# Kernel tuning notes

Hardware: AMD Instinct MI355X
Metric: run time of the kernel (lower is better)

## Reference

```python
import jax, jax.numpy as jnp
import numpy as np

N, E = 50000, 640000          # nodes, edges
F_IN, HID, CLS = 128, 128, 64  # feature dims


def setup_inputs() -> dict:
    key = jax.random.key(0)
    ks = jax.random.split(key, 12)
    x = jax.random.normal(ks[0], (N, F_IN), dtype=jnp.float32)
    edge_index = jax.random.randint(ks[1], (2, E), 0, N, dtype=jnp.int32)
    s_in = 1.0 / np.sqrt(F_IN)
    s_h = 1.0 / np.sqrt(HID)
    return {
        "x": x,
        "edge_index": edge_index,
        "W0": jax.random.normal(ks[2], (F_IN, HID), jnp.float32) * s_in,
        "b0": jnp.zeros((HID,), jnp.float32),
        "W1": jax.random.normal(ks[3], (HID, HID), jnp.float32) * s_h,
        "b1": jnp.zeros((HID,), jnp.float32),
        "W2": jax.random.normal(ks[4], (HID, HID), jnp.float32) * s_h,
        "b2": jnp.zeros((HID,), jnp.float32),
        "W_lin": jax.random.normal(ks[5], (HID, CLS), jnp.float32) * s_h,
        "b_lin": jnp.zeros((CLS,), jnp.float32),
    }


def reference(x, edge_index, W0, b0, W1, b1, W2, b2, W_lin, b_lin):
    # GCNConv (PyG defaults): out = D^-1/2 (A + I) D^-1/2 (x @ W) + b
    row, col = edge_index[0], edge_index[1]  # source -> target
    # degree with self-loop (graph is fixed across layers, compute norms once)
    deg = jnp.zeros((N,), x.dtype).at[col].add(1.0) + 1.0
    dinv = jax.lax.rsqrt(deg)                 # deg >= 1, safe
    enorm = (dinv[row] * dinv[col])[:, None]  # [E,1] edge norm
    snorm = (dinv * dinv)[:, None]            # [N,1] self-loop norm

    def conv(h, W, b):
        h = h @ W                                             # [N,HID]
        agg = jnp.zeros_like(h).at[col].add(h[row] * enorm)   # neighbor agg
        return agg + h * snorm + b                            # + self loop + bias

    h = jax.nn.relu(conv(x, W0, b0))
    h = jax.nn.relu(conv(h, W1, b1))
    h = jax.nn.relu(conv(h, W2, b2))
    return h @ W_lin + b_lin
```

## Files before the change

kernel.cpp:

```cpp
#include <hip/hip_runtime.h>
#include <hip/hip_fp16.h>

#define N_NODES 50000
#define HID 128
#define CLS 64

#define NBINS 196
#define NBLK 256
#define LBUF_CAP 4096
#define WTOT 57344
#define GEMM0_BLOCKS 782
#define AROW 136

typedef __attribute__((ext_vector_type(8))) _Float16 f16x8;
typedef __attribute__((ext_vector_type(4))) float f32x4;

__global__ __launch_bounds__(256) void hist_wsplit_kernel(
    const int* __restrict__ col, int* __restrict__ hist,
    const float* __restrict__ W0, const float* __restrict__ W1,
    const float* __restrict__ W2, const float* __restrict__ Wl,
    __half* __restrict__ o0h, __half* __restrict__ o0l,
    __half* __restrict__ o1h, __half* __restrict__ o1l,
    __half* __restrict__ o2h, __half* __restrict__ o2l,
    __half* __restrict__ o3h, __half* __restrict__ o3l,
    int E, int chunk) {
    int widx = blockIdx.x * 256 + threadIdx.x;
    if (widx < WTOT) {
        const float* W;
        __half *oh, *ol;
        int NCdim, local;
        if (widx < 16384)      { W = W0; oh = o0h; ol = o0l; NCdim = 128; local = widx; }
        else if (widx < 32768) { W = W1; oh = o1h; ol = o1l; NCdim = 128; local = widx - 16384; }
        else if (widx < 49152) { W = W2; oh = o2h; ol = o2l; NCdim = 128; local = widx - 32768; }
        else                   { W = Wl; oh = o3h; ol = o3l; NCdim = 64;  local = widx - 49152; }
        int nn = local >> 7;
        int k = local & 127;
        float v = W[(size_t)k * NCdim + nn];
        __half h = __float2half_rn(v);
        oh[local] = h;
        ol[local] = __float2half_rn(v - __half2float(h));
    }
    __shared__ int h[NBINS];
    for (int i = threadIdx.x; i < NBINS; i += 256) h[i] = 0;
    __syncthreads();
    int b = blockIdx.x;
    int beg = b * chunk;
    int end = min(E, beg + chunk);
    if (beg < end) {
        int vend = beg + ((end - beg) & ~3);
        for (int i = beg + threadIdx.x * 4; i < vend; i += 1024) {
            int4 c4 = *(const int4*)(col + i);
            atomicAdd(&h[c4.x >> 8], 1);
            atomicAdd(&h[c4.y >> 8], 1);
            atomicAdd(&h[c4.z >> 8], 1);
            atomicAdd(&h[c4.w >> 8], 1);
        }
        int i = vend + threadIdx.x;
        if (i < end) atomicAdd(&h[col[i] >> 8], 1);
    }
    __syncthreads();
    for (int i = threadIdx.x; i < NBINS; i += 256)
        hist[i * NBLK + b] = h[i];
}

__global__ __launch_bounds__(256) void binscan_kernel(
    const int* __restrict__ hist, int* __restrict__ cursorBase,
    int* __restrict__ binTotal) {
    __shared__ int ss[256];
    int bin = blockIdx.x, t = threadIdx.x;
    int v = hist[bin * NBLK + t];
    ss[t] = v;
    __syncthreads();
#pragma unroll
    for (int off = 1; off < 256; off <<= 1) {
        int u = (t >= off) ? ss[t - off] : 0;
        __syncthreads();
        ss[t] += u;
        __syncthreads();
    }
    cursorBase[bin * NBLK + t] = ss[t] - v;
    if (t == 255) binTotal[bin] = ss[255];
}

__global__ __launch_bounds__(256) void scatter_kernel(
    const int* __restrict__ row, const int* __restrict__ col,
    const int* __restrict__ binTotal, const int* __restrict__ cursorBase,
    int* __restrict__ binBase_g,
    unsigned short* __restrict__ sbuf_src, unsigned char* __restrict__ sbuf_c,
    int E, int chunk) {
    __shared__ int ss[256];
    __shared__ int cur[NBINS];
    int b = blockIdx.x, t = threadIdx.x;
    int v = (t < NBINS) ? binTotal[t] : 0;
    ss[t] = v;
    __syncthreads();
#pragma unroll
    for (int off = 1; off < 256; off <<= 1) {
        int u = (t >= off) ? ss[t - off] : 0;
        __syncthreads();
        ss[t] += u;
        __syncthreads();
    }
    int myBase = ss[t] - v;
    if (t < NBINS) cur[t] = myBase + cursorBase[t * NBLK + b];
    if (b == 0) {
        if (t < NBINS) binBase_g[t] = myBase;
        if (t == 0) binBase_g[NBINS] = E;
    }
    __syncthreads();
    int beg = b * chunk;
    int end = min(E, beg + chunk);
    if (beg >= end) return;
    int vend = beg + ((end - beg) & ~3);
    for (int i = beg + t * 4; i < vend; i += 1024) {
        int4 c4 = *(const int4*)(col + i);
        int4 r4 = *(const int4*)(row + i);
        int p;
        p = atomicAdd(&cur[c4.x >> 8], 1); sbuf_src[p] = (unsigned short)r4.x; sbuf_c[p] = (unsigned char)(c4.x & 255);
        p = atomicAdd(&cur[c4.y >> 8], 1); sbuf_src[p] = (unsigned short)r4.y; sbuf_c[p] = (unsigned char)(c4.y & 255);
        p = atomicAdd(&cur[c4.z >> 8], 1); sbuf_src[p] = (unsigned short)r4.z; sbuf_c[p] = (unsigned char)(c4.z & 255);
        p = atomicAdd(&cur[c4.w >> 8], 1); sbuf_src[p] = (unsigned short)r4.w; sbuf_c[p] = (unsigned char)(c4.w & 255);
    }
    int i = vend + t;
    if (i < end) {
        int c = col[i];
        int p = atomicAdd(&cur[c >> 8], 1);
        sbuf_src[p] = (unsigned short)row[i];
        sbuf_c[p] = (unsigned char)(c & 255);
    }
}

__device__ __forceinline__ void gemm0_lds_body(
    const float* __restrict__ x, const __half* __restrict__ Bh,
    const __half* __restrict__ Bl, __half* __restrict__ C, int M,
    int rowBase, __half* Als ) {
    int t = threadIdx.x;
#pragma unroll
    for (int it = 0; it < 8; ++it) {
        int idx = it * 256 + t;
        int r = idx >> 5;
        int cq = idx & 31;
        int grow = rowBase + r;
        if (grow < M) {
            float4 v = *(const float4*)(x + (size_t)grow * 128 + cq * 4);
            __half2 h0 = __float22half2_rn(make_float2(v.x, v.y));
            __half2 h1 = __float22half2_rn(make_float2(v.z, v.w));
            __half2* dst = (__half2*)(Als + r * AROW + cq * 4);
            dst[0] = h0;
            dst[1] = h1;
        }
    }
    __syncthreads();
    int wave = t >> 6;
    int lane = t & 63;
    int m0 = rowBase + (wave << 4);
    if (m0 >= M) return;
    int mr = lane & 15;
    int kq = (lane >> 4) << 3;
    const __half* bh = Bh + (size_t)mr * 128 + kq;
    const __half* bl = Bl + (size_t)mr * 128 + kq;
    const __half* arow = Als + (wave * 16 + mr) * AROW + kq;

    f32x4 acc[8];
#pragma unroll
    for (int tt = 0; tt < 8; ++tt) acc[tt] = (f32x4){0.f, 0.f, 0.f, 0.f};
#pragma unroll
    for (int kc = 0; kc < 128; kc += 32) {
        f16x8 a = *(const f16x8*)(arow + kc);
#pragma unroll
        for (int tt = 0; tt < 8; ++tt) {
            f16x8 wh = *(const f16x8*)(bh + (size_t)tt * 16 * 128 + kc);
            f16x8 wl = *(const f16x8*)(bl + (size_t)tt * 16 * 128 + kc);
            acc[tt] = __builtin_amdgcn_mfma_f32_16x16x32_f16(a, wh, acc[tt], 0, 0, 0);
            acc[tt] = __builtin_amdgcn_mfma_f32_16x16x32_f16(a, wl, acc[tt], 0, 0, 0);
        }
    }
    int r0 = m0 + ((lane >> 4) << 2);
    int cc = lane & 15;
#pragma unroll
    for (int tt = 0; tt < 8; ++tt)
#pragma unroll
        for (int r = 0; r < 4; ++r) {
            if (r0 + r >= M) break;
            C[(size_t)(r0 + r) * 128 + tt * 16 + cc] =
                __float2half_rn(acc[tt][r]);
        }
}

__global__ __launch_bounds__(256) void csrplace_gemm0_kernel(
    const int* __restrict__ binBase,
    const unsigned short* __restrict__ sbuf_src, const unsigned char* __restrict__ sbuf_c,
    float* __restrict__ dinv, int* __restrict__ row_ptr,
    unsigned short* __restrict__ csr_src,
    const float* __restrict__ x, const __half* __restrict__ W0h,
    const __half* __restrict__ W0l, __half* __restrict__ h2, int n, int E) {
    __shared__ __align__(16) int smem[4864];
    int b = blockIdx.x;
    if (b >= NBINS) {
        gemm0_lds_body(x, W0h, W0l, h2, n, (b - NBINS) * 64, (__half*)smem);
        return;
    }
    int* lcnt = smem;
    int* lcur = smem + 256;
    int* ss   = smem + 512;
    int* lbuf = smem + 768;
    int t = threadIdx.x;
    lcnt[t] = 0;
    __syncthreads();
    int beg = binBase[b], end = binBase[b + 1];
    for (int j = beg + t; j < end; j += 256)
        atomicAdd(&lcnt[sbuf_c[j]], 1);
    __syncthreads();
    int deg = lcnt[t];
    int node = b * 256 + t;
    if (node < n) dinv[node] = rsqrtf((float)deg + 1.0f);
    ss[t] = deg;
    __syncthreads();
#pragma unroll
    for (int off = 1; off < 256; off <<= 1) {
        int u = (t >= off) ? ss[t - off] : 0;
        __syncthreads();
        ss[t] += u;
        __syncthreads();
    }
    int excl = ss[t] - deg;
    lcur[t] = excl;
    int total = ss[255];
    if (node < n) row_ptr[node] = beg + excl;
    if (b == 0 && t == 0) row_ptr[n] = E;
    __syncthreads();
    for (int j = beg + t; j < end; j += 256) {
        int c = sbuf_c[j];
        int pos = atomicAdd(&lcur[c], 1);
        lbuf[pos] = sbuf_src[j];
    }
    __syncthreads();
    for (int j = t; j < total; j += 256)
        csr_src[beg + j] = (unsigned short)lbuf[j];
}

template<int NC, bool HEAD>
__global__ __launch_bounds__(256) void agg_gemm_kernel(
    const __half* __restrict__ h2, const int* __restrict__ row_ptr,
    const unsigned short* __restrict__ csr_src, const float* __restrict__ dinv,
    const float* __restrict__ bias,
    const __half* __restrict__ Bh, const __half* __restrict__ Bl,
    const float* __restrict__ gbias, void* __restrict__ Cv, int n) {
    __shared__ __half Als[16][AROW];
    int wave = threadIdx.x >> 6;
    int lane = threadIdx.x & 63;
    int m0 = blockIdx.x << 4;

    int g = lane >> 4;
    int l16 = lane & 15;
    int baseLane = lane & 48;
    int lr = (wave << 2) + g;
    int wid = m0 + lr;
    const __half* hrow = h2 + (l16 << 3);

    if (wid < n) {
        int beg = row_ptr[wid];
        int end = row_ptr[wid + 1];
        float dv = dinv[wid];
        float acc[8];
#pragma unroll
        for (int i = 0; i < 8; ++i) acc[i] = 0.f;

        for (int base = beg; base < end; base += 16) {
            int cnt = end - base;
            if (cnt > 16) cnt = 16;
            int msrc = 0;
            float mw = 0.f;
            if (l16 < cnt) {
                msrc = csr_src[base + l16];
                mw = dinv[msrc] * dv;
            }
            int j = 0;
            for (; j + 4 <= cnt; j += 4) {
                int s0 = __shfl(msrc, baseLane + j);
                int s1 = __shfl(msrc, baseLane + j + 1);
                int s2 = __shfl(msrc, baseLane + j + 2);
                int s3 = __shfl(msrc, baseLane + j + 3);
                float w0 = __shfl(mw, baseLane + j);
                float w1 = __shfl(mw, baseLane + j + 1);
                float w2 = __shfl(mw, baseLane + j + 2);
                float w3 = __shfl(mw, baseLane + j + 3);
                f16x8 v0 = *(const f16x8*)(hrow + ((size_t)s0 << 7));
                f16x8 v1 = *(const f16x8*)(hrow + ((size_t)s1 << 7));
                f16x8 v2 = *(const f16x8*)(hrow + ((size_t)s2 << 7));
                f16x8 v3 = *(const f16x8*)(hrow + ((size_t)s3 << 7));
#pragma unroll
                for (int i = 0; i < 8; ++i) {
                    acc[i] = fmaf((float)v0[i], w0, acc[i]);
                    acc[i] = fmaf((float)v1[i], w1, acc[i]);
                    acc[i] = fmaf((float)v2[i], w2, acc[i]);
                    acc[i] = fmaf((float)v3[i], w3, acc[i]);
                }
            }
            for (; j + 2 <= cnt; j += 2) {
                int s0 = __shfl(msrc, baseLane + j);
                int s1 = __shfl(msrc, baseLane + j + 1);
                float w0 = __shfl(mw, baseLane + j);
                float w1 = __shfl(mw, baseLane + j + 1);
                f16x8 v0 = *(const f16x8*)(hrow + ((size_t)s0 << 7));
                f16x8 v1 = *(const f16x8*)(hrow + ((size_t)s1 << 7));
#pragma unroll
                for (int i = 0; i < 8; ++i) {
                    acc[i] = fmaf((float)v0[i], w0, acc[i]);
                    acc[i] = fmaf((float)v1[i], w1, acc[i]);
                }
            }
            if (j < cnt) {
                int s0 = __shfl(msrc, baseLane + j);
                float w0 = __shfl(mw, baseLane + j);
                f16x8 v0 = *(const f16x8*)(hrow + ((size_t)s0 << 7));
#pragma unroll
                for (int i = 0; i < 8; ++i)
                    acc[i] = fmaf((float)v0[i], w0, acc[i]);
            }
        }
        float sn = dv * dv;
        f16x8 sv = *(const f16x8*)(hrow + ((size_t)wid << 7));
        float4 ba = *(const float4*)(bias + (l16 << 3));
        float4 bb = *(const float4*)(bias + (l16 << 3) + 4);
        float o[8];
#pragma unroll
        for (int i = 0; i < 8; ++i) o[i] = fmaf((float)sv[i], sn, acc[i]);
        o[0] += ba.x; o[1] += ba.y; o[2] += ba.z; o[3] += ba.w;
        o[4] += bb.x; o[5] += bb.y; o[6] += bb.z; o[7] += bb.w;
        f16x8 pk;
#pragma unroll
        for (int i = 0; i < 8; ++i) pk[i] = (_Float16)fmaxf(o[i], 0.f);
        *(f16x8*)&Als[lr][l16 << 3] = pk;
    }
    __syncthreads();

    constexpr int NT = NC / 16;
    constexpr int TPW = NT / 4;
    int mr = lane & 15;
    int kq = (lane >> 4) << 3;
    const __half* bh = Bh + (size_t)mr * 128 + kq;
    const __half* bl = Bl + (size_t)mr * 128 + kq;

    f32x4 acc[TPW];
#pragma unroll
    for (int t = 0; t < TPW; ++t) acc[t] = (f32x4){0.f, 0.f, 0.f, 0.f};
#pragma unroll
    for (int kc = 0; kc < 128; kc += 32) {
        f16x8 a = *(const f16x8*)&Als[mr][kq + kc];
#pragma unroll
        for (int t = 0; t < TPW; ++t) {
            int tile = wave * TPW + t;
            f16x8 wh = *(const f16x8*)(bh + (size_t)tile * 16 * 128 + kc);
            f16x8 wl = *(const f16x8*)(bl + (size_t)tile * 16 * 128 + kc);
            acc[t] = __builtin_amdgcn_mfma_f32_16x16x32_f16(a, wh, acc[t], 0, 0, 0);
            acc[t] = __builtin_amdgcn_mfma_f32_16x16x32_f16(a, wl, acc[t], 0, 0, 0);
        }
    }
    int r0 = m0 + ((lane >> 4) << 2);
    int cc = lane & 15;
#pragma unroll
    for (int t = 0; t < TPW; ++t) {
        int tile = wave * TPW + t;
        float bsv = HEAD ? gbias[tile * 16 + cc] : 0.f;
#pragma unroll
        for (int r = 0; r < 4; ++r) {
            if (r0 + r >= n) break;
            size_t idx = (size_t)(r0 + r) * NC + tile * 16 + cc;
            float val = acc[t][r] + bsv;
            if (HEAD)
                ((float*)Cv)[idx] = val;
            else
                ((__half*)Cv)[idx] = __float2half_rn(val);
        }
    }
}

extern "C" void kernel_launch(void* const* d_in, const int* in_sizes, int n_in,
                              void* d_out, int out_size, void* d_ws, size_t ws_size,
                              hipStream_t stream) {
    const float* x  = (const float*)d_in[0];
    const int* ei   = (const int*)d_in[1];
    const float* W0 = (const float*)d_in[2];
    const float* b0 = (const float*)d_in[3];
    const float* W1 = (const float*)d_in[4];
    const float* b1 = (const float*)d_in[5];
    const float* W2 = (const float*)d_in[6];
    const float* b2 = (const float*)d_in[7];
    const float* Wl = (const float*)d_in[8];
    const float* bl = (const float*)d_in[9];
    float* out = (float*)d_out;

    const int N = N_NODES;
    const int E = in_sizes[1] / 2;
    const int* row = ei;
    const int* col = ei + E;
    const int chunk = (((E + NBLK - 1) / NBLK) + 3) & ~3;

    char* ws = (char*)d_ws;
    auto alloc = [&](size_t bytes) {
        char* p = ws;
        ws += (bytes + 255) & ~(size_t)255;
        return p;
    };
    int*   hist      = (int*)alloc((size_t)NBINS * NBLK * 4);
    int*   cursorBase= (int*)alloc((size_t)NBINS * NBLK * 4);
    int*   binTotal  = (int*)alloc((size_t)NBINS * 4);
    int*   binBase   = (int*)alloc((size_t)(NBINS + 1) * 4);
    unsigned short* sbuf_src = (unsigned short*)alloc((size_t)E * 2);
    unsigned char*  sbuf_c   = (unsigned char*)alloc((size_t)E);
    int*   row_ptr = (int*)alloc((size_t)(N + 1) * 4);
    float* dinv    = (float*)alloc((size_t)N * 4);
    unsigned short* csr_src = (unsigned short*)alloc((size_t)E * 2);
    __half* h2a    = (__half*)alloc((size_t)N * HID * 2);
    __half* h2b    = (__half*)alloc((size_t)N * HID * 2);
    __half* Wt_h[4];
    __half* Wt_l[4];
    for (int i = 0; i < 3; ++i) {
        Wt_h[i] = (__half*)alloc((size_t)HID * HID * 2);
        Wt_l[i] = (__half*)alloc((size_t)HID * HID * 2);
    }
    Wt_h[3] = (__half*)alloc((size_t)CLS * HID * 2);
    Wt_l[3] = (__half*)alloc((size_t)CLS * HID * 2);

    hist_wsplit_kernel<<<NBLK, 256, 0, stream>>>(col, hist, W0, W1, W2, Wl,
        Wt_h[0], Wt_l[0], Wt_h[1], Wt_l[1], Wt_h[2], Wt_l[2], Wt_h[3], Wt_l[3], E, chunk);
    binscan_kernel<<<NBINS, 256, 0, stream>>>(hist, cursorBase, binTotal);
    scatter_kernel<<<NBLK, 256, 0, stream>>>(row, col, binTotal, cursorBase,
        binBase, sbuf_src, sbuf_c, E, chunk);
    csrplace_gemm0_kernel<<<NBINS + GEMM0_BLOCKS, 256, 0, stream>>>(
        binBase, sbuf_src, sbuf_c, dinv, row_ptr, csr_src,
        x, Wt_h[0], Wt_l[0], h2a, N, E);

    const int fusedBlocks = (N + 15) / 16;

    agg_gemm_kernel<128, false><<<fusedBlocks, 256, 0, stream>>>(
        h2a, row_ptr, csr_src, dinv, b0, Wt_h[1], Wt_l[1], nullptr, h2b, N);
    agg_gemm_kernel<128, false><<<fusedBlocks, 256, 0, stream>>>(
        h2b, row_ptr, csr_src, dinv, b1, Wt_h[2], Wt_l[2], nullptr, h2a, N);
    agg_gemm_kernel<64, true><<<fusedBlocks, 256, 0, stream>>>(
        h2a, row_ptr, csr_src, dinv, b2, Wt_h[3], Wt_l[3], bl, out, N);
}
```

Before: 268.2 us.

## Fuse CSR build stages into persistent mega-kernel with grid barriers

Merges the histogram, bin scan, scatter and CSR placement kernels into one launch that separates its stages with software grid barriers (an atomic counter plus spin), while extra blocks run the first GEMM concurrently, each handling up to two tiles. The weight split moves to its own small kernel and the barrier counter is reset with a memset. This removes several kernel launch gaps and lets GEMM0 overlap the graph preprocessing. It relies on all 256 prep blocks being co-resident, which is not guaranteed when 1024 blocks are launched, so it risks deadlock, and the spin-waits hold compute units.

```diff
diff --git a/kernel.cpp b/kernel.cpp
--- a/kernel.cpp
+++ b/kernel.cpp
@@ -9,125 +9,47 @@
 #define NBLK 256
 #define LBUF_CAP 4096
 #define WTOT 57344
-#define GEMM0_BLOCKS 782
+#define WSPLIT_BLOCKS 224
+#define GEMM0_TILES 782
+#define MEGA_BLOCKS 1024
+#define GEMM0_MEGA (MEGA_BLOCKS - NBLK)
 #define AROW 136
 
 typedef __attribute__((ext_vector_type(8))) _Float16 f16x8;
 typedef __attribute__((ext_vector_type(4))) float f32x4;
 
-__global__ __launch_bounds__(256) void hist_wsplit_kernel(
-    const int* __restrict__ col, int* __restrict__ hist,
+__global__ __launch_bounds__(256) void wsplit_kernel(
     const float* __restrict__ W0, const float* __restrict__ W1,
     const float* __restrict__ W2, const float* __restrict__ Wl,
     __half* __restrict__ o0h, __half* __restrict__ o0l,
     __half* __restrict__ o1h, __half* __restrict__ o1l,
     __half* __restrict__ o2h, __half* __restrict__ o2l,
-    __half* __restrict__ o3h, __half* __restrict__ o3l,
-    int E, int chunk) {
+    __half* __restrict__ o3h, __half* __restrict__ o3l) {
     int widx = blockIdx.x * 256 + threadIdx.x;
-    if (widx < WTOT) {
-        const float* W;
-        __half *oh, *ol;
-        int NCdim, local;
-        if (widx < 16384)      { W = W0; oh = o0h; ol = o0l; NCdim = 128; local = widx; }
-        else if (widx < 32768) { W = W1; oh = o1h; ol = o1l; NCdim = 128; local = widx - 16384; }
-        else if (widx < 49152) { W = W2; oh = o2h; ol = o2l; NCdim = 128; local = widx - 32768; }
-        else                   { W = Wl; oh = o3h; ol = o3l; NCdim = 64;  local = widx - 49152; }
-        int nn = local >> 7;
-        int k = local & 127;
-        float v = W[(size_t)k * NCdim + nn];
-        __half h = __float2half_rn(v);
-        oh[local] = h;
-        ol[local] = __float2half_rn(v - __half2float(h));
-    }
-    __shared__ int h[NBINS];
-    for (int i = threadIdx.x; i < NBINS; i += 256) h[i] = 0;
+    const float* W;
+    __half *oh, *ol;
+    int NCdim, local;
+    if (widx < 16384)      { W = W0; oh = o0h; ol = o0l; NCdim = 128; local = widx; }
+    else if (widx < 32768) { W = W1; oh = o1h; ol = o1l; NCdim = 128; local = widx - 16384; }
+    else if (widx < 49152) { W = W2; oh = o2h; ol = o2l; NCdim = 128; local = widx - 32768; }
+    else                   { W = Wl; oh = o3h; ol = o3l; NCdim = 64;  local = widx - 49152; }
+    int nn = local >> 7;
+    int k = local & 127;
+    float v = W[(size_t)k * NCdim + nn];
+    __half h = __float2half_rn(v);
+    oh[local] = h;
+    ol[local] = __float2half_rn(v - __half2float(h));
+}
+
+__device__ __forceinline__ void prep_barrier(int* bar, int target) {
     __syncthreads();
-    int b = blockIdx.x;
-    int beg = b * chunk;
-    int end = min(E, beg + chunk);
-    if (beg < end) {
-        int vend = beg + ((end - beg) & ~3);
-        for (int i = beg + threadIdx.x * 4; i < vend; i += 1024) {
-            int4 c4 = *(const int4*)(col + i);
-            atomicAdd(&h[c4.x >> 8], 1);
-            atomicAdd(&h[c4.y >> 8], 1);
-            atomicAdd(&h[c4.z >> 8], 1);
-            atomicAdd(&h[c4.w >> 8], 1);
-        }
-        int i = vend + threadIdx.x;
-        if (i < end) atomicAdd(&h[col[i] >> 8], 1);
+    if (threadIdx.x == 0) {
+        __threadfence();
+        atomicAdd(bar, 1);
+        while (__hip_atomic_load(bar, __ATOMIC_ACQUIRE,
+                                 __HIP_MEMORY_SCOPE_AGENT) < target) {}
     }
     __syncthreads();
-    for (int i = threadIdx.x; i < NBINS; i += 256)
-        hist[i * NBLK + b] = h[i];
-}
-
-__global__ __launch_bounds__(256) void binscan_kernel(
-    const int* __restrict__ hist, int* __restrict__ cursorBase,
-    int* __restrict__ binTotal) {
-    __shared__ int ss[256];
-    int bin = blockIdx.x, t = threadIdx.x;
-    int v = hist[bin * NBLK + t];
-    ss[t] = v;
-    __syncthreads();
-#pragma unroll
-    for (int off = 1; off < 256; off <<= 1) {
-        int u = (t >= off) ? ss[t - off] : 0;
-        __syncthreads();
-        ss[t] += u;
-        __syncthreads();
-    }
-    cursorBase[bin * NBLK + t] = ss[t] - v;
-    if (t == 255) binTotal[bin] = ss[255];
-}
-
-__global__ __launch_bounds__(256) void scatter_kernel(
-    const int* __restrict__ row, const int* __restrict__ col,
-    const int* __restrict__ binTotal, const int* __restrict__ cursorBase,
-    int* __restrict__ binBase_g,
-    unsigned short* __restrict__ sbuf_src, unsigned char* __restrict__ sbuf_c,
-    int E, int chunk) {
-    __shared__ int ss[256];
-    __shared__ int cur[NBINS];
-    int b = blockIdx.x, t = threadIdx.x;
-    int v = (t < NBINS) ? binTotal[t] : 0;
-    ss[t] = v;
-    __syncthreads();
-#pragma unroll
-    for (int off = 1; off < 256; off <<= 1) {
-        int u = (t >= off) ? ss[t - off] : 0;
-        __syncthreads();
-        ss[t] += u;
-        __syncthreads();
-    }
-    int myBase = ss[t] - v;
-    if (t < NBINS) cur[t] = myBase + cursorBase[t * NBLK + b];
-    if (b == 0) {
-        if (t < NBINS) binBase_g[t] = myBase;
-        if (t == 0) binBase_g[NBINS] = E;
-    }
-    __syncthreads();
-    int beg = b * chunk;
-    int end = min(E, beg + chunk);
-    if (beg >= end) return;
-    int vend = beg + ((end - beg) & ~3);
-    for (int i = beg + t * 4; i < vend; i += 1024) {
-        int4 c4 = *(const int4*)(col + i);
-        int4 r4 = *(const int4*)(row + i);
-        int p;
-        p = atomicAdd(&cur[c4.x >> 8], 1); sbuf_src[p] = (unsigned short)r4.x; sbuf_c[p] = (unsigned char)(c4.x & 255);
-        p = atomicAdd(&cur[c4.y >> 8], 1); sbuf_src[p] = (unsigned short)r4.y; sbuf_c[p] = (unsigned char)(c4.y & 255);
-        p = atomicAdd(&cur[c4.z >> 8], 1); sbuf_src[p] = (unsigned short)r4.z; sbuf_c[p] = (unsigned char)(c4.z & 255);
-        p = atomicAdd(&cur[c4.w >> 8], 1); sbuf_src[p] = (unsigned short)r4.w; sbuf_c[p] = (unsigned char)(c4.w & 255);
-    }
-    int i = vend + t;
-    if (i < end) {
-        int c = col[i];
-        int p = atomicAdd(&cur[c >> 8], 1);
-        sbuf_src[p] = (unsigned short)row[i];
-        sbuf_c[p] = (unsigned char)(c & 255);
-    }
 }
 
 __device__ __forceinline__ void gemm0_lds_body(
@@ -187,56 +109,153 @@
         }
 }
 
-__global__ __launch_bounds__(256) void csrplace_gemm0_kernel(
-    const int* __restrict__ binBase,
-    const unsigned short* __restrict__ sbuf_src, const unsigned char* __restrict__ sbuf_c,
+__global__ __launch_bounds__(256) void prep_gemm0_mega_kernel(
+    const int* __restrict__ row, const int* __restrict__ col,
+    int* __restrict__ hist, int* __restrict__ cursorBase,
+    int* __restrict__ binTotal, int* __restrict__ binBase,
+    unsigned short* __restrict__ sbuf_src, unsigned char* __restrict__ sbuf_c,
     float* __restrict__ dinv, int* __restrict__ row_ptr,
-    unsigned short* __restrict__ csr_src,
+    unsigned short* __restrict__ csr_src, int* bar,
     const float* __restrict__ x, const __half* __restrict__ W0h,
-    const __half* __restrict__ W0l, __half* __restrict__ h2, int n, int E) {
+    const __half* __restrict__ W0l, __half* __restrict__ h2,
+    int n, int E, int chunk) {
     __shared__ __align__(16) int smem[4864];
     int b = blockIdx.x;
-    if (b >= NBINS) {
-        gemm0_lds_body(x, W0h, W0l, h2, n, (b - NBINS) * 64, (__half*)smem);
+    int t = threadIdx.x;
+
+    if (b >= NBLK) {
+        int g0 = b - NBLK;
+        gemm0_lds_body(x, W0h, W0l, h2, n, g0 * 64, (__half*)smem);
+        if (g0 + GEMM0_MEGA < GEMM0_TILES) {
+            __syncthreads();
+            gemm0_lds_body(x, W0h, W0l, h2, n, (g0 + GEMM0_MEGA) * 64, (__half*)smem);
+        }
         return;
     }
-    int* lcnt = smem;
-    int* lcur = smem + 256;
-    int* ss   = smem + 512;
-    int* lbuf = smem + 768;
-    int t = threadIdx.x;
-    lcnt[t] = 0;
-    __syncthreads();
-    int beg = binBase[b], end = binBase[b + 1];
-    for (int j = beg + t; j < end; j += 256)
-        atomicAdd(&lcnt[sbuf_c[j]], 1);
-    __syncthreads();
-    int deg = lcnt[t];
-    int node = b * 256 + t;
-    if (node < n) dinv[node] = rsqrtf((float)deg + 1.0f);
-    ss[t] = deg;
-    __syncthreads();
-#pragma unroll
-    for (int off = 1; off < 256; off <<= 1) {
-        int u = (t >= off) ? ss[t - off] : 0;
-        __syncthreads();
-        ss[t] += u;
-        __syncthreads();
-    }
-    int excl = ss[t] - deg;
-    lcur[t] = excl;
-    int total = ss[255];
-    if (node < n) row_ptr[node] = beg + excl;
-    if (b == 0 && t == 0) row_ptr[n] = E;
-    __syncthreads();
-    for (int j = beg + t; j < end; j += 256) {
-        int c = sbuf_c[j];
-        int pos = atomicAdd(&lcur[c], 1);
-        lbuf[pos] = sbuf_src[j];
-    }
-    __syncthreads();
-    for (int j = t; j < total; j += 256)
-        csr_src[beg + j] = (unsigned short)lbuf[j];
+
+    {
+        int* h = smem;
+        for (int i = t; i < NBINS; i += 256) h[i] = 0;
+        __syncthreads();
+        int beg = b * chunk;
+        int end = min(E, beg + chunk);
+        if (beg < end) {
+            int vend = beg + ((end - beg) & ~3);
+            for (int i = beg + t * 4; i < vend; i += 1024) {
+                int4 c4 = *(const int4*)(col + i);
+                atomicAdd(&h[c4.x >> 8], 1);
+                atomicAdd(&h[c4.y >> 8], 1);
+                atomicAdd(&h[c4.z >> 8], 1);
+                atomicAdd(&h[c4.w >> 8], 1);
+            }
+            int i = vend + t;
+            if (i < end) atomicAdd(&h[col[i] >> 8], 1);
+        }
+        __syncthreads();
+        for (int i = t; i < NBINS; i += 256)
+            hist[i * NBLK + b] = h[i];
+    }
+    prep_barrier(bar, NBLK);
+
+    if (b < NBINS) {
+        int* ss = smem;
+        int v = hist[b * NBLK + t];
+        ss[t] = v;
+        __syncthreads();
+#pragma unroll
+        for (int off = 1; off < 256; off <<= 1) {
+            int u = (t >= off) ? ss[t - off] : 0;
+            __syncthreads();
+            ss[t] += u;
+            __syncthreads();
+        }
+        cursorBase[b * NBLK + t] = ss[t] - v;
+        if (t == 255) binTotal[b] = ss[255];
+    }
+    prep_barrier(bar, 2 * NBLK);
+
+    {
+        int* ss  = smem;
+        int* cur = smem + 256;
+        int v = (t < NBINS) ? binTotal[t] : 0;
+        ss[t] = v;
+        __syncthreads();
+#pragma unroll
+        for (int off = 1; off < 256; off <<= 1) {
+            int u = (t >= off) ? ss[t - off] : 0;
+            __syncthreads();
+            ss[t] += u;
+            __syncthreads();
+        }
+        int myBase = ss[t] - v;
+        if (t < NBINS) cur[t] = myBase + cursorBase[t * NBLK + b];
+        if (b == 0) {
+            if (t < NBINS) binBase[t] = myBase;
+            if (t == 0) binBase[NBINS] = E;
+        }
+        __syncthreads();
+        int beg = b * chunk;
+        int end = min(E, beg + chunk);
+        if (beg < end) {
+            int vend = beg + ((end - beg) & ~3);
+            for (int i = beg + t * 4; i < vend; i += 1024) {
+                int4 c4 = *(const int4*)(col + i);
+                int4 r4 = *(const int4*)(row + i);
+                int p;
+                p = atomicAdd(&cur[c4.x >> 8], 1); sbuf_src[p] = (unsigned short)r4.x; sbuf_c[p] = (unsigned char)(c4.x & 255);
+                p = atomicAdd(&cur[c4.y >> 8], 1); sbuf_src[p] = (unsigned short)r4.y; sbuf_c[p] = (unsigned char)(c4.y & 255);
+                p = atomicAdd(&cur[c4.z >> 8], 1); sbuf_src[p] = (unsigned short)r4.z; sbuf_c[p] = (unsigned char)(c4.z & 255);
+                p = atomicAdd(&cur[c4.w >> 8], 1); sbuf_src[p] = (unsigned short)r4.w; sbuf_c[p] = (unsigned char)(c4.w & 255);
+            }
+            int i = vend + t;
+            if (i < end) {
+                int c = col[i];
+                int p = atomicAdd(&cur[c >> 8], 1);
+                sbuf_src[p] = (unsigned short)row[i];
+                sbuf_c[p] = (unsigned char)(c & 255);
+            }
+        }
+    }
+    prep_barrier(bar, 3 * NBLK);
+
+    if (b < NBINS) {
+        int* lcnt = smem;
+        int* lcur = smem + 256;
+        int* ss   = smem + 512;
+        int* lbuf = smem + 768;
+        lcnt[t] = 0;
+        __syncthreads();
+        int beg = binBase[b], end = binBase[b + 1];
+        for (int j = beg + t; j < end; j += 256)
+            atomicAdd(&lcnt[sbuf_c[j]], 1);
+        __syncthreads();
+        int deg = lcnt[t];
+        int node = b * 256 + t;
+        if (node < n) dinv[node] = rsqrtf((float)deg + 1.0f);
+        ss[t] = deg;
+        __syncthreads();
+#pragma unroll
+        for (int off = 1; off < 256; off <<= 1) {
+            int u = (t >= off) ? ss[t - off] : 0;
+            __syncthreads();
+            ss[t] += u;
+            __syncthreads();
+        }
+        int excl = ss[t] - deg;
+        lcur[t] = excl;
+        int total = ss[255];
+        if (node < n) row_ptr[node] = beg + excl;
+        if (b == 0 && t == 0) row_ptr[n] = E;
+        __syncthreads();
+        for (int j = beg + t; j < end; j += 256) {
+            int c = sbuf_c[j];
+            int pos = atomicAdd(&lcur[c], 1);
+            lbuf[pos] = sbuf_src[j];
+        }
+        __syncthreads();
+        for (int j = t; j < total; j += 256)
+            csr_src[beg + j] = (unsigned short)lbuf[j];
+    }
 }
 
 template<int NC, bool HEAD>
@@ -407,6 +426,7 @@
     int*   cursorBase= (int*)alloc((size_t)NBINS * NBLK * 4);
     int*   binTotal  = (int*)alloc((size_t)NBINS * 4);
     int*   binBase   = (int*)alloc((size_t)(NBINS + 1) * 4);
+    int*   bar       = (int*)alloc(256);
     unsigned short* sbuf_src = (unsigned short*)alloc((size_t)E * 2);
     unsigned char*  sbuf_c   = (unsigned char*)alloc((size_t)E);
     int*   row_ptr = (int*)alloc((size_t)(N + 1) * 4);
@@ -423,14 +443,14 @@
     Wt_h[3] = (__half*)alloc((size_t)CLS * HID * 2);
     Wt_l[3] = (__half*)alloc((size_t)CLS * HID * 2);
 
-    hist_wsplit_kernel<<<NBLK, 256, 0, stream>>>(col, hist, W0, W1, W2, Wl,
-        Wt_h[0], Wt_l[0], Wt_h[1], Wt_l[1], Wt_h[2], Wt_l[2], Wt_h[3], Wt_l[3], E, chunk);
-    binscan_kernel<<<NBINS, 256, 0, stream>>>(hist, cursorBase, binTotal);
-    scatter_kernel<<<NBLK, 256, 0, stream>>>(row, col, binTotal, cursorBase,
-        binBase, sbuf_src, sbuf_c, E, chunk);
-    csrplace_gemm0_kernel<<<NBINS + GEMM0_BLOCKS, 256, 0, stream>>>(
-        binBase, sbuf_src, sbuf_c, dinv, row_ptr, csr_src,
-        x, Wt_h[0], Wt_l[0], h2a, N, E);
+    hipMemsetAsync(bar, 0, 256, stream);
+
+    wsplit_kernel<<<WSPLIT_BLOCKS, 256, 0, stream>>>(W0, W1, W2, Wl,
+        Wt_h[0], Wt_l[0], Wt_h[1], Wt_l[1], Wt_h[2], Wt_l[2], Wt_h[3], Wt_l[3]);
+
+    prep_gemm0_mega_kernel<<<MEGA_BLOCKS, 256, 0, stream>>>(
+        row, col, hist, cursorBase, binTotal, binBase, sbuf_src, sbuf_c,
+        dinv, row_ptr, csr_src, bar, x, Wt_h[0], Wt_l[0], h2a, N, E, chunk);
 
     const int fusedBlocks = (N + 15) / 16;
 
```

Result: slower. 347.8 us (+29.7%).
